# Optimization experiments

Measured on AMD Instinct MI355X. Metric: run time of the kernel, lower is better.

The kernel has to match this reference:

```python
import jax, jax.numpy as jnp
import numpy as np

B, S, D, H = 2, 2048, 1024, 16


def setup_inputs() -> dict:
    key = jax.random.key(0)
    ks = jax.random.split(key, 8)
    wscale = 1.0 / np.sqrt(D)  # ~xavier for square matrices
    return {
        "q": jax.random.normal(ks[0], (B, S, D), jnp.float32),
        "k": jax.random.normal(ks[1], (B, S, D), jnp.float32),
        "v": jax.random.normal(ks[2], (B, S, D), jnp.float32),
        "mask": jnp.tril(jnp.ones((S, S), jnp.int32))[None, None, :, :],  # [1,1,S,S] causal
        "Wq": jax.random.normal(ks[3], (D, D), jnp.float32) * wscale,
        "bq": jnp.zeros((D,), jnp.float32),
        "Wk": jax.random.normal(ks[4], (D, D), jnp.float32) * wscale,
        "bk": jnp.zeros((D,), jnp.float32),
        "Wv": jax.random.normal(ks[5], (D, D), jnp.float32) * wscale,
        "bv": jnp.zeros((D,), jnp.float32),
        "Wo": jax.random.normal(ks[6], (D, D), jnp.float32) * wscale,
        "bo": jnp.zeros((D,), jnp.float32),
    }


def reference(q, k, v, mask, Wq, bq, Wk, bk, Wv, bv, Wo, bo):
    batch_size, seq_len = q.shape[0], q.shape[1]
    qp = q @ Wq + bq
    kp = k @ Wk + bk
    vp = v @ Wv + bv
    qkv = jnp.concatenate([qp, kp, vp], axis=2)          # [B,S,3D]
    qkv = jnp.reshape(qkv, (batch_size, seq_len, H, -1), order='F')  # faithful Fortran-order head split
    qkv = qkv.transpose(0, 2, 1, 3)                      # [B,H,S,3*hd]
    qh, kh, vh = jnp.array_split(qkv, 3, axis=-1)        # each [B,H,S,hd]
    scores = qh @ jnp.swapaxes(kh, -2, -1) / kh.shape[-1] ** 0.5  # [B,H,S,S]
    scores = jnp.where(mask == 0, -9e15, scores)
    attention = jax.nn.softmax(scores, axis=-1)
    values = attention @ vh                              # [B,H,S,hd]
    values = values.transpose(0, 2, 1, 3).reshape(batch_size, seq_len, D)
    out = values @ Wo + bo
    return (out, attention)
```

## Files before the change

kernel.cpp:

```cpp
#include <hip/hip_runtime.h>
#include <stdint.h>

#define B_ 2
#define S_ 2048
#define D_ 1024
#define H_ 16
#define HD_ 64
#define BS_ 4096

typedef __bf16 bf16_t;
typedef __attribute__((ext_vector_type(8))) __bf16 bf16x8;
typedef __attribute__((ext_vector_type(4))) float f32x4;

#define VMCNT0 asm volatile("s_waitcnt vmcnt(0)" ::: "memory")
#define LGKMCNT0 asm volatile("s_waitcnt lgkmcnt(0)" ::: "memory")

__device__ __forceinline__ void barrier_raw() {
  asm volatile("" ::: "memory");
  __builtin_amdgcn_s_barrier();
  asm volatile("" ::: "memory");
}

__device__ __forceinline__ bf16_t f2bf(float f) {
  union { float f; uint32_t u; } v; v.f = f;
  uint32_t r = v.u + 0x7FFFu + ((v.u >> 16) & 1u);
  union { uint16_t u; bf16_t b; } o; o.u = (uint16_t)(r >> 16);
  return o.b;
}

__device__ __forceinline__ void gload_lds16(const void* g, void* l) {
  __builtin_amdgcn_global_load_lds((const __attribute__((address_space(1))) void*)g,
                                   (__attribute__((address_space(3))) void*)l,
                                   16, 0, 0);
}

__device__ __forceinline__ void stage64(const bf16_t* __restrict__ g, int gstride,
                                        bf16_t* lds, int wave, int lane) {
  #pragma unroll
  for (int i = 0; i < 2; ++i) {
    int lin = (wave * 2 + i) * 64 + lane;
    int row = lin >> 3, c = lin & 7;
    gload_lds16(g + (size_t)row * gstride + ((c ^ (row & 7)) << 3), (char*)lds + lin * 16);
  }
}

__device__ __forceinline__ void stage128(const bf16_t* __restrict__ g, int gstride,
                                         bf16_t* lds, int wave, int lane) {
  #pragma unroll
  for (int i = 0; i < 4; ++i) {
    int lin = (wave * 4 + i) * 64 + lane;
    int row = lin >> 3, c = lin & 7;
    gload_lds16(g + (size_t)row * gstride + ((c ^ (row & 7)) << 3), (char*)lds + lin * 16);
  }
}

__device__ __forceinline__ bf16x8 frag64(const bf16_t* lds, int row, int chunk) {
  return *(const bf16x8*)((const char*)lds + row * 128 + ((chunk ^ (row & 7)) << 4));
}

__global__ __launch_bounds__(256) void to_bf16_3_kernel(const float* __restrict__ q,
                                                        const float* __restrict__ k,
                                                        const float* __restrict__ v,
                                                        bf16_t* __restrict__ qb,
                                                        bf16_t* __restrict__ kb,
                                                        bf16_t* __restrict__ vb) {
  const int which = blockIdx.y;
  const float* in = which == 0 ? q : which == 1 ? k : v;
  bf16_t* out = which == 0 ? qb : which == 1 ? kb : vb;
  int i = (blockIdx.x * 256 + threadIdx.x) * 8;
  const float4* p = (const float4*)(in + i);
  float4 a = p[0], b = p[1];
  bf16x8 o;
  o[0] = f2bf(a.x); o[1] = f2bf(a.y); o[2] = f2bf(a.z); o[3] = f2bf(a.w);
  o[4] = f2bf(b.x); o[5] = f2bf(b.y); o[6] = f2bf(b.z); o[7] = f2bf(b.w);
  *(bf16x8*)(out + i) = o;
}

__global__ __launch_bounds__(256) void conv_weight4_kernel(const float* __restrict__ Wq,
                                                           const float* __restrict__ Wk,
                                                           const float* __restrict__ Wv,
                                                           const float* __restrict__ Wo,
                                                           bf16_t* __restrict__ wt_base) {
  const int which = blockIdx.z;
  const float* w = which == 0 ? Wq : which == 1 ? Wk : which == 2 ? Wv : Wo;
  bf16_t* wt = wt_base + (size_t)which * D_ * D_;
  const int permute = (which < 3) ? 1 : 0;
  const float scale = (which == 0) ? 0.125f : 1.0f;

  __shared__ float tile[64][65];
  int d0 = blockIdx.x * 64, o0 = blockIdx.y * 64;
  #pragma unroll
  for (int it = 0; it < 16; ++it) {
    int e = it * 256 + threadIdx.x;
    int r = e >> 6, c = e & 63;
    tile[r][c] = w[(size_t)(d0 + r) * D_ + o0 + c];
  }
  __syncthreads();
  #pragma unroll
  for (int it = 0; it < 16; ++it) {
    int e = it * 256 + threadIdx.x;
    int dd = e & 63, oo = e >> 6;
    int o = o0 + oo;
    int np = permute ? ((o & 15) * 64 + (o >> 4)) : o;
    wt[(size_t)np * D_ + d0 + dd] = f2bf(tile[dd][oo] * scale);
  }
}

__global__ __launch_bounds__(256) void perm_bias_kernel(const float* __restrict__ bq,
                                                        const float* __restrict__ bk,
                                                        const float* __restrict__ bv,
                                                        float* __restrict__ out) {
  int i = blockIdx.x * 256 + threadIdx.x;
  if (i >= 3 * D_) return;
  int which = i >> 10, n = i & 1023;
  int src = (n >> 6) + ((n & 63) << 4);
  const float* b = which == 0 ? bq : (which == 1 ? bk : bv);
  out[i] = b[src] * (which == 0 ? 0.125f : 1.0f);
}

__global__ __launch_bounds__(256) void gemm_qkv_kernel(const bf16_t* __restrict__ Aq,
                                                       const bf16_t* __restrict__ Ak,
                                                       const bf16_t* __restrict__ Av,
                                                       const bf16_t* __restrict__ Bt,
                                                       const float* __restrict__ bias,
                                                       bf16_t* __restrict__ Oq,
                                                       bf16_t* __restrict__ Ok,
                                                       bf16_t* __restrict__ Ov) {
  __shared__ bf16_t As[128 * 64];
  __shared__ bf16_t Bs[128 * 64];
  const int tid = threadIdx.x, wave = tid >> 6, lane = tid & 63;
  const int wm = wave >> 1, wn = wave & 1;
  const int lrow = lane & 15, kgrp = lane >> 4;
  const int row0 = blockIdx.x * 128;
  const int which = blockIdx.y >> 3;
  const int col0 = (blockIdx.y & 7) * 128;
  const bf16_t* A = which == 0 ? Aq : which == 1 ? Ak : Av;
  bf16_t* O = which == 0 ? Oq : which == 1 ? Ok : Ov;
  const bf16_t* Brow = Bt + (size_t)(which * 1024 + col0) * 1024;
  const float* bs = bias + which * 1024 + col0;

  f32x4 acc[4][4];
  #pragma unroll
  for (int i = 0; i < 4; ++i)
    #pragma unroll
    for (int j = 0; j < 4; ++j) acc[i][j] = (f32x4){0.f, 0.f, 0.f, 0.f};

  for (int k0 = 0; k0 < 1024; k0 += 64) {
    __syncthreads();
    stage128(A + (size_t)row0 * 1024 + k0, 1024, As, wave, lane);
    stage128(Brow + k0, 1024, Bs, wave, lane);
    VMCNT0;
    __syncthreads();
    #pragma unroll
    for (int kk = 0; kk < 2; ++kk) {
      bf16x8 af[4], bfv[4];
      #pragma unroll
      for (int mi = 0; mi < 4; ++mi) af[mi] = frag64(As, wm * 64 + mi * 16 + lrow, kk * 4 + kgrp);
      #pragma unroll
      for (int nj = 0; nj < 4; ++nj) bfv[nj] = frag64(Bs, wn * 64 + nj * 16 + lrow, kk * 4 + kgrp);
      #pragma unroll
      for (int mi = 0; mi < 4; ++mi)
        #pragma unroll
        for (int nj = 0; nj < 4; ++nj)
          acc[mi][nj] = __builtin_amdgcn_mfma_f32_16x16x32_bf16(af[mi], bfv[nj], acc[mi][nj], 0, 0, 0);
    }
  }

  #pragma unroll
  for (int mi = 0; mi < 4; ++mi)
    #pragma unroll
    for (int nj = 0; nj < 4; ++nj) {
      const int col = wn * 64 + nj * 16 + lrow;
      const float bv = bs[col];
      #pragma unroll
      for (int r = 0; r < 4; ++r) {
        const int row = row0 + wm * 64 + mi * 16 + kgrp * 4 + r;
        O[(size_t)row * 1024 + col0 + col] = f2bf(acc[mi][nj][r] + bv);
      }
    }
}

__global__ __launch_bounds__(256) void gemm_out_kernel(const bf16_t* __restrict__ A,
                                                       const bf16_t* __restrict__ Bt,
                                                       const float* __restrict__ bias,
                                                       float* __restrict__ Cout) {
  __shared__ bf16_t As[128 * 64];
  __shared__ bf16_t Bs[64 * 64];
  const int tid = threadIdx.x, wave = tid >> 6, lane = tid & 63;
  const int wm = wave >> 1, wn = wave & 1;
  const int lrow = lane & 15, kgrp = lane >> 4;
  const int row0 = blockIdx.x * 128;
  const int col0 = blockIdx.y * 64;

  f32x4 acc[4][2];
  #pragma unroll
  for (int i = 0; i < 4; ++i)
    #pragma unroll
    for (int j = 0; j < 2; ++j) acc[i][j] = (f32x4){0.f, 0.f, 0.f, 0.f};

  for (int k0 = 0; k0 < 1024; k0 += 64) {
    __syncthreads();
    stage128(A + (size_t)row0 * 1024 + k0, 1024, As, wave, lane);
    stage64(Bt + (size_t)col0 * 1024 + k0, 1024, Bs, wave, lane);
    VMCNT0;
    __syncthreads();
    #pragma unroll
    for (int kk = 0; kk < 2; ++kk) {
      bf16x8 af[4], bfv[2];
      #pragma unroll
      for (int mi = 0; mi < 4; ++mi) af[mi] = frag64(As, wm * 64 + mi * 16 + lrow, kk * 4 + kgrp);
      #pragma unroll
      for (int nj = 0; nj < 2; ++nj) bfv[nj] = frag64(Bs, wn * 32 + nj * 16 + lrow, kk * 4 + kgrp);
      #pragma unroll
      for (int mi = 0; mi < 4; ++mi)
        #pragma unroll
        for (int nj = 0; nj < 2; ++nj)
          acc[mi][nj] = __builtin_amdgcn_mfma_f32_16x16x32_bf16(af[mi], bfv[nj], acc[mi][nj], 0, 0, 0);
    }
  }

  #pragma unroll
  for (int mi = 0; mi < 4; ++mi)
    #pragma unroll
    for (int nj = 0; nj < 2; ++nj) {
      const int col = col0 + wn * 32 + nj * 16 + lrow;
      const float bv = bias[col];
      #pragma unroll
      for (int r = 0; r < 4; ++r) {
        const int row = row0 + wm * 64 + mi * 16 + kgrp * 4 + r;
        Cout[(size_t)row * 1024 + col] = acc[mi][nj][r] + bv;
      }
    }
}

__global__ __launch_bounds__(256) void transpose_v_kernel(const bf16_t* __restrict__ Vp,
                                                          bf16_t* __restrict__ Vt) {
  __shared__ bf16_t t[64][80];
  const int st = blockIdx.x, bh = blockIdx.y;
  const int b = bh >> 4, h = bh & 15;
  const int tid = threadIdx.x;
  #pragma unroll
  for (int i = 0; i < 2; ++i) {
    int lin = i * 256 + tid;
    int r = lin >> 3, c = (lin & 7) * 8;
    bf16x8 v8 = *(const bf16x8*)(Vp + ((size_t)(b * S_ + st * 64 + r)) * D_ + h * HD_ + c);
    *(bf16x8*)&t[r][c] = v8;
  }
  __syncthreads();
  #pragma unroll
  for (int i = 0; i < 2; ++i) {
    int lin = i * 256 + tid;
    int f = lin >> 3, c = (lin & 7) * 8;
    bf16x8 o;
    #pragma unroll
    for (int e = 0; e < 8; ++e) o[e] = t[c + e][f];
    *(bf16x8*)(Vt + ((size_t)bh * HD_ + f) * S_ + st * 64 + c) = o;
  }
}

__global__ __launch_bounds__(256) void attn_kernel(const bf16_t* __restrict__ Q,
                                                   const bf16_t* __restrict__ K,
                                                   const bf16_t* __restrict__ Vt,
                                                   float* __restrict__ attn_out,
                                                   bf16_t* __restrict__ values) {
  __shared__ bf16_t Qs[64 * 64];
  __shared__ bf16_t KsB[2][64 * 64];
  __shared__ bf16_t VtsB[2][64 * 64];
  __shared__ bf16_t Ps[4][16 * 72];

  const int tid = threadIdx.x;
  const int wave = tid >> 6, lane = tid & 63;
  const int lrow = lane & 15, kgrp = lane >> 4;
  const int bh = blockIdx.y, b = bh >> 4, h = bh & 15;
  const size_t base = (size_t)b * S_ * D_ + (size_t)h * HD_;
  const size_t vbase = (size_t)bh * HD_ * S_;

  #pragma unroll 1
  for (int half = 0; half < 2; ++half) {
    const int qt = (half == 0) ? (int)blockIdx.x : 31 - (int)blockIdx.x;
    const int qr0 = qt * 64;

    barrier_raw();
    stage64(Q + base + (size_t)qr0 * D_, D_, Qs, wave, lane);
    stage64(K + base, D_, KsB[0], wave, lane);
    VMCNT0; barrier_raw();

    bf16x8 aq[2];
    #pragma unroll
    for (int kk = 0; kk < 2; ++kk) aq[kk] = frag64(Qs, wave * 16 + lrow, kk * 4 + kgrp);

    float psum[4] = {0.f, 0.f, 0.f, 0.f};
    for (int kj = 0; kj <= qt; ++kj) {
      if (kj < qt) stage64(K + base + (size_t)(kj + 1) * 64 * D_, D_, KsB[(kj + 1) & 1], wave, lane);
      const bf16_t* Kc = KsB[kj & 1];
      f32x4 s[4];
      #pragma unroll
      for (int nj = 0; nj < 4; ++nj) {
        s[nj] = (f32x4){0.f, 0.f, 0.f, 0.f};
        #pragma unroll
        for (int kk = 0; kk < 2; ++kk)
          s[nj] = __builtin_amdgcn_mfma_f32_16x16x32_bf16(
              aq[kk], frag64(Kc, nj * 16 + lrow, kk * 4 + kgrp), s[nj], 0, 0, 0);
      }
      if (kj == qt) {
        #pragma unroll
        for (int nj = 0; nj < 4; ++nj)
          #pragma unroll
          for (int r = 0; r < 4; ++r) {
            int lrq = wave * 16 + kgrp * 4 + r;
            int lck = nj * 16 + lrow;
            psum[r] += (lck > lrq) ? 0.f : __expf(s[nj][r]);
          }
      } else {
        #pragma unroll
        for (int nj = 0; nj < 4; ++nj)
          #pragma unroll
          for (int r = 0; r < 4; ++r) psum[r] += __expf(s[nj][r]);
      }
      VMCNT0; barrier_raw();
    }

    float rl[4];
    #pragma unroll
    for (int r = 0; r < 4; ++r) {
      float t = psum[r];
      #pragma unroll
      for (int off = 1; off < 16; off <<= 1) t += __shfl_xor(t, off);
      rl[r] = 1.0f / t;
    }

    f32x4 o[4];
    #pragma unroll
    for (int nj = 0; nj < 4; ++nj) o[nj] = (f32x4){0.f, 0.f, 0.f, 0.f};

    stage64(K + base, D_, KsB[0], wave, lane);
    stage64(Vt + vbase, S_, VtsB[0], wave, lane);
    VMCNT0; barrier_raw();

    for (int kj = 0; kj <= qt; ++kj) {
      if (kj < qt) {
        stage64(K + base + (size_t)(kj + 1) * 64 * D_, D_, KsB[(kj + 1) & 1], wave, lane);
        stage64(Vt + vbase + (kj + 1) * 64, S_, VtsB[(kj + 1) & 1], wave, lane);
      }
      __builtin_amdgcn_sched_barrier(0);
      const bf16_t* Kc = KsB[kj & 1];
      const bf16_t* Vc = VtsB[kj & 1];
      f32x4 s[4];
      #pragma unroll
      for (int nj = 0; nj < 4; ++nj) {
        s[nj] = (f32x4){0.f, 0.f, 0.f, 0.f};
        #pragma unroll
        for (int kk = 0; kk < 2; ++kk)
          s[nj] = __builtin_amdgcn_mfma_f32_16x16x32_bf16(
              aq[kk], frag64(Kc, nj * 16 + lrow, kk * 4 + kgrp), s[nj], 0, 0, 0);
      }
      float* gpb = attn_out + ((size_t)bh * S_ + qr0 + wave * 16 + kgrp * 4) * S_ + kj * 64;
      #pragma unroll
      for (int nj = 0; nj < 4; ++nj)
        #pragma unroll
        for (int r = 0; r < 4; ++r) {
          int lrq = wave * 16 + kgrp * 4 + r;
          int lck = nj * 16 + lrow;
          float p = __expf(s[nj][r]) * rl[r];
          if (kj == qt && lck > lrq) p = 0.f;
          gpb[(size_t)r * S_ + nj * 16 + lrow] = p;
          Ps[wave][(kgrp * 4 + r) * 72 + nj * 16 + lrow] = f2bf(p);
        }
      LGKMCNT0;

      bf16x8 pa[2];
      #pragma unroll
      for (int kk = 0; kk < 2; ++kk)
        pa[kk] = *(const bf16x8*)((const char*)&Ps[wave][0] + lrow * 144 + (kk * 4 + kgrp) * 16);
      #pragma unroll
      for (int nj = 0; nj < 4; ++nj)
        #pragma unroll
        for (int kk = 0; kk < 2; ++kk)
          o[nj] = __builtin_amdgcn_mfma_f32_16x16x32_bf16(
              pa[kk], frag64(Vc, nj * 16 + lrow, kk * 4 + kgrp), o[nj], 0, 0, 0);

      asm volatile("s_waitcnt vmcnt(16)" ::: "memory");
      barrier_raw();
    }

    {
      const int cstart = (qt + 1) * 64;
      if (cstart < S_) {
        int r = tid >> 2;
        float4 z = make_float4(0.f, 0.f, 0.f, 0.f);
        float* rowp = attn_out + ((size_t)bh * S_ + qr0 + r) * S_;
        for (int c = cstart + (tid & 3) * 4; c < S_; c += 16) *(float4*)(rowp + c) = z;
      }
    }

    #pragma unroll
    for (int nj = 0; nj < 4; ++nj)
      #pragma unroll
      for (int r = 0; r < 4; ++r) {
        int grow = qr0 + wave * 16 + kgrp * 4 + r;
        values[(size_t)(b * S_ + grow) * D_ + h * HD_ + nj * 16 + lrow] = f2bf(o[nj][r]);
      }
  }
}

extern "C" void kernel_launch(void* const* d_in, const int* in_sizes, int n_in,
                              void* d_out, int out_size, void* d_ws, size_t ws_size,
                              hipStream_t stream) {
  const float* q  = (const float*)d_in[0];
  const float* k  = (const float*)d_in[1];
  const float* v  = (const float*)d_in[2];
  const float* Wq = (const float*)d_in[4];
  const float* bq = (const float*)d_in[5];
  const float* Wk = (const float*)d_in[6];
  const float* bk = (const float*)d_in[7];
  const float* Wv = (const float*)d_in[8];
  const float* bv = (const float*)d_in[9];
  const float* Wo = (const float*)d_in[10];
  const float* bo = (const float*)d_in[11];

  char* ws = (char*)d_ws;
  bf16_t* qb    = (bf16_t*)ws;
  bf16_t* kb    = qb + (size_t)BS_ * D_;
  bf16_t* vb    = kb + (size_t)BS_ * D_;
  bf16_t* Wqt   = vb + (size_t)BS_ * D_;
  bf16_t* Wkt   = Wqt + (size_t)D_ * D_;
  bf16_t* Wvt   = Wkt + (size_t)D_ * D_;
  bf16_t* Wot   = Wvt + (size_t)D_ * D_;
  float*  bias3 = (float*)(Wot + (size_t)D_ * D_);
  bf16_t* Qp    = (bf16_t*)(bias3 + 3 * D_);
  bf16_t* Kp    = Qp + (size_t)BS_ * D_;
  bf16_t* Vp    = Kp + (size_t)BS_ * D_;
  bf16_t* Vt    = qb;
  bf16_t* Val   = kb;

  to_bf16_3_kernel<<<dim3(2048, 3), 256, 0, stream>>>(q, k, v, qb, kb, vb);
  conv_weight4_kernel<<<dim3(16, 16, 4), 256, 0, stream>>>(Wq, Wk, Wv, Wo, Wqt);
  perm_bias_kernel<<<12, 256, 0, stream>>>(bq, bk, bv, bias3);

  gemm_qkv_kernel<<<dim3(32, 24), 256, 0, stream>>>(qb, kb, vb, Wqt, bias3, Qp, Kp, Vp);
  transpose_v_kernel<<<dim3(32, 32), 256, 0, stream>>>(Vp, Vt);

  float* attn_out = (float*)d_out + (size_t)BS_ * D_;
  attn_kernel<<<dim3(16, 32), 256, 0, stream>>>(Qp, Kp, Vt, attn_out, Val);

  gemm_out_kernel<<<dim3(32, 16), 256, 0, stream>>>(Val, Wot, bo, (float*)d_out);
}
```

Before: 326.8 us.

## Load attention K/V fragments directly to registers and use exp2 with folded scale

The attention kernel no longer stages Q, K and V^T tiles through shared memory with block barriers. Each wave now loads its MFMA fragments straight from global memory into double-buffered registers, and the PV accumulate is software-pipelined one step behind the score computation. The Q weight and bias scale is changed to fold log2(e), so exp2 can replace expf. This removes LDS traffic and barrier stalls, at the cost of more VGPRs and redundant global loads across the four waves, which share K/V only through the cache.

Measured after the change: 413.1 us. 1.26x slower.

```diff
diff --git a/kernel.cpp b/kernel.cpp
--- a/kernel.cpp
+++ b/kernel.cpp
@@ -15,11 +15,7 @@
 #define VMCNT0 asm volatile("s_waitcnt vmcnt(0)" ::: "memory")
 #define LGKMCNT0 asm volatile("s_waitcnt lgkmcnt(0)" ::: "memory")
 
-__device__ __forceinline__ void barrier_raw() {
-  asm volatile("" ::: "memory");
-  __builtin_amdgcn_s_barrier();
-  asm volatile("" ::: "memory");
-}
+#define EXP2F(x) __builtin_amdgcn_exp2f(x)
 
 __device__ __forceinline__ bf16_t f2bf(float f) {
   union { float f; uint32_t u; } v; v.f = f;
@@ -85,7 +81,7 @@
   const float* w = which == 0 ? Wq : which == 1 ? Wk : which == 2 ? Wv : Wo;
   bf16_t* wt = wt_base + (size_t)which * D_ * D_;
   const int permute = (which < 3) ? 1 : 0;
-  const float scale = (which == 0) ? 0.125f : 1.0f;
+  const float scale = (which == 0) ? 0.18033688f : 1.0f;
 
   __shared__ float tile[64][65];
   int d0 = blockIdx.x * 64, o0 = blockIdx.y * 64;
@@ -115,7 +111,7 @@
   int which = i >> 10, n = i & 1023;
   int src = (n >> 6) + ((n & 63) << 4);
   const float* b = which == 0 ? bq : (which == 1 ? bk : bv);
-  out[i] = b[src] * (which == 0 ? 0.125f : 1.0f);
+  out[i] = b[src] * (which == 0 ? 0.18033688f : 1.0f);
 }
 
 __global__ __launch_bounds__(256) void gemm_qkv_kernel(const bf16_t* __restrict__ Aq,
@@ -263,63 +259,100 @@
                                                    const bf16_t* __restrict__ Vt,
                                                    float* __restrict__ attn_out,
                                                    bf16_t* __restrict__ values) {
-  __shared__ bf16_t Qs[64 * 64];
-  __shared__ bf16_t KsB[2][64 * 64];
-  __shared__ bf16_t VtsB[2][64 * 64];
   __shared__ bf16_t Ps[4][16 * 72];
-
   const int tid = threadIdx.x;
   const int wave = tid >> 6, lane = tid & 63;
   const int lrow = lane & 15, kgrp = lane >> 4;
   const int bh = blockIdx.y, b = bh >> 4, h = bh & 15;
   const size_t base = (size_t)b * S_ * D_ + (size_t)h * HD_;
   const size_t vbase = (size_t)bh * HD_ * S_;
+  bf16_t* psw = &Ps[wave][0];
+
+#define LDK(kj_, kf_)                                                          \
+  {                                                                            \
+    const bf16_t* p_ = kp + (size_t)(kj_) * 64 * D_;                           \
+    _Pragma("unroll") for (int nj = 0; nj < 4; ++nj) {                         \
+      kf_[nj * 2] = *(const bf16x8*)(p_ + (size_t)nj * 16 * D_);               \
+      kf_[nj * 2 + 1] = *(const bf16x8*)(p_ + (size_t)nj * 16 * D_ + 32);      \
+    }                                                                          \
+  }
+#define LDV(kj_, vf_)                                                          \
+  {                                                                            \
+    const bf16_t* p_ = vp + (kj_) * 64;                                        \
+    _Pragma("unroll") for (int nj = 0; nj < 4; ++nj) {                         \
+      vf_[nj * 2] = *(const bf16x8*)(p_ + (size_t)nj * 16 * S_);               \
+      vf_[nj * 2 + 1] = *(const bf16x8*)(p_ + (size_t)nj * 16 * S_ + 32);      \
+    }                                                                          \
+  }
+#define QKS(kf_)                                                               \
+  _Pragma("unroll") for (int nj = 0; nj < 4; ++nj) {                           \
+    s[nj] = (f32x4){0.f, 0.f, 0.f, 0.f};                                       \
+    s[nj] = __builtin_amdgcn_mfma_f32_16x16x32_bf16(aq0, kf_[nj * 2], s[nj], 0, 0, 0); \
+    s[nj] = __builtin_amdgcn_mfma_f32_16x16x32_bf16(aq1, kf_[nj * 2 + 1], s[nj], 0, 0, 0); \
+  }
+#define P1BODY(kf_, kj_)                                                       \
+  {                                                                            \
+    f32x4 s[4];                                                                \
+    QKS(kf_)                                                                   \
+    _Pragma("unroll") for (int nj = 0; nj < 4; ++nj)                           \
+      _Pragma("unroll") for (int r = 0; r < 4; ++r) {                          \
+        float e = EXP2F(s[nj][r]);                                             \
+        if ((kj_) == qt && (nj * 16 + lrow) > (wave * 16 + kgrp * 4 + r)) e = 0.f; \
+        psum[r] += e;                                                          \
+      }                                                                        \
+  }
+#define PVACC(vf_)                                                             \
+  {                                                                            \
+    LGKMCNT0;                                                                  \
+    bf16x8 pa0 = *(const bf16x8*)((const char*)psw + lrow * 144 + kgrp * 16);  \
+    bf16x8 pa1 = *(const bf16x8*)((const char*)psw + lrow * 144 + (4 + kgrp) * 16); \
+    _Pragma("unroll") for (int nj = 0; nj < 4; ++nj) {                         \
+      o[nj] = __builtin_amdgcn_mfma_f32_16x16x32_bf16(pa0, vf_[nj * 2], o[nj], 0, 0, 0); \
+      o[nj] = __builtin_amdgcn_mfma_f32_16x16x32_bf16(pa1, vf_[nj * 2 + 1], o[nj], 0, 0, 0); \
+    }                                                                          \
+  }
+#define P2BODY(kc_, kn_, vc_, vn_, kj_)                                        \
+  {                                                                            \
+    if ((kj_) < qt) LDK((kj_) + 1, kn_);                                       \
+    LDV((kj_), vn_);                                                           \
+    f32x4 s[4];                                                                \
+    QKS(kc_)                                                                   \
+    if ((kj_) > 0) PVACC(vc_)                                                  \
+    float* gpb = attn_out + ((size_t)bh * S_ + qr0 + wave * 16 + kgrp * 4) * S_ + (kj_) * 64; \
+    _Pragma("unroll") for (int nj = 0; nj < 4; ++nj)                           \
+      _Pragma("unroll") for (int r = 0; r < 4; ++r) {                          \
+        float p = EXP2F(s[nj][r]) * rl[r];                                     \
+        if ((kj_) == qt && (nj * 16 + lrow) > (wave * 16 + kgrp * 4 + r)) p = 0.f; \
+        gpb[(size_t)r * S_ + nj * 16 + lrow] = p;                              \
+        psw[(kgrp * 4 + r) * 72 + nj * 16 + lrow] = f2bf(p);                   \
+      }                                                                        \
+  }
 
   #pragma unroll 1
   for (int half = 0; half < 2; ++half) {
     const int qt = (half == 0) ? (int)blockIdx.x : 31 - (int)blockIdx.x;
     const int qr0 = qt * 64;
 
-    barrier_raw();
-    stage64(Q + base + (size_t)qr0 * D_, D_, Qs, wave, lane);
-    stage64(K + base, D_, KsB[0], wave, lane);
-    VMCNT0; barrier_raw();
-
-    bf16x8 aq[2];
-    #pragma unroll
-    for (int kk = 0; kk < 2; ++kk) aq[kk] = frag64(Qs, wave * 16 + lrow, kk * 4 + kgrp);
+    const bf16_t* qp = Q + base + (size_t)(qr0 + wave * 16 + lrow) * D_ + kgrp * 8;
+    bf16x8 aq0 = *(const bf16x8*)qp;
+    bf16x8 aq1 = *(const bf16x8*)(qp + 32);
+    const bf16_t* kp = K + base + (size_t)lrow * D_ + kgrp * 8;
+    const bf16_t* vp = Vt + vbase + (size_t)lrow * S_ + kgrp * 8;
 
     float psum[4] = {0.f, 0.f, 0.f, 0.f};
-    for (int kj = 0; kj <= qt; ++kj) {
-      if (kj < qt) stage64(K + base + (size_t)(kj + 1) * 64 * D_, D_, KsB[(kj + 1) & 1], wave, lane);
-      const bf16_t* Kc = KsB[kj & 1];
-      f32x4 s[4];
-      #pragma unroll
-      for (int nj = 0; nj < 4; ++nj) {
-        s[nj] = (f32x4){0.f, 0.f, 0.f, 0.f};
-        #pragma unroll
-        for (int kk = 0; kk < 2; ++kk)
-          s[nj] = __builtin_amdgcn_mfma_f32_16x16x32_bf16(
-              aq[kk], frag64(Kc, nj * 16 + lrow, kk * 4 + kgrp), s[nj], 0, 0, 0);
-      }
-      if (kj == qt) {
-        #pragma unroll
-        for (int nj = 0; nj < 4; ++nj)
-          #pragma unroll
-          for (int r = 0; r < 4; ++r) {
-            int lrq = wave * 16 + kgrp * 4 + r;
-            int lck = nj * 16 + lrow;
-            psum[r] += (lck > lrq) ? 0.f : __expf(s[nj][r]);
-          }
-      } else {
-        #pragma unroll
-        for (int nj = 0; nj < 4; ++nj)
-          #pragma unroll
-          for (int r = 0; r < 4; ++r) psum[r] += __expf(s[nj][r]);
-      }
-      VMCNT0; barrier_raw();
-    }
-
+    {
+      bf16x8 kA[8], kB[8];
+      LDK(0, kA);
+      int kj = 0;
+      while (true) {
+        if (kj < qt) LDK(kj + 1, kB);
+        P1BODY(kA, kj);
+        if (++kj > qt) break;
+        if (kj < qt) LDK(kj + 1, kA);
+        P1BODY(kB, kj);
+        if (++kj > qt) break;
+      }
+    }
     float rl[4];
     #pragma unroll
     for (int r = 0; r < 4; ++r) {
@@ -332,55 +365,17 @@
     f32x4 o[4];
     #pragma unroll
     for (int nj = 0; nj < 4; ++nj) o[nj] = (f32x4){0.f, 0.f, 0.f, 0.f};
-
-    stage64(K + base, D_, KsB[0], wave, lane);
-    stage64(Vt + vbase, S_, VtsB[0], wave, lane);
-    VMCNT0; barrier_raw();
-
-    for (int kj = 0; kj <= qt; ++kj) {
-      if (kj < qt) {
-        stage64(K + base + (size_t)(kj + 1) * 64 * D_, D_, KsB[(kj + 1) & 1], wave, lane);
-        stage64(Vt + vbase + (kj + 1) * 64, S_, VtsB[(kj + 1) & 1], wave, lane);
-      }
-      __builtin_amdgcn_sched_barrier(0);
-      const bf16_t* Kc = KsB[kj & 1];
-      const bf16_t* Vc = VtsB[kj & 1];
-      f32x4 s[4];
-      #pragma unroll
-      for (int nj = 0; nj < 4; ++nj) {
-        s[nj] = (f32x4){0.f, 0.f, 0.f, 0.f};
-        #pragma unroll
-        for (int kk = 0; kk < 2; ++kk)
-          s[nj] = __builtin_amdgcn_mfma_f32_16x16x32_bf16(
-              aq[kk], frag64(Kc, nj * 16 + lrow, kk * 4 + kgrp), s[nj], 0, 0, 0);
-      }
-      float* gpb = attn_out + ((size_t)bh * S_ + qr0 + wave * 16 + kgrp * 4) * S_ + kj * 64;
-      #pragma unroll
-      for (int nj = 0; nj < 4; ++nj)
-        #pragma unroll
-        for (int r = 0; r < 4; ++r) {
-          int lrq = wave * 16 + kgrp * 4 + r;
-          int lck = nj * 16 + lrow;
-          float p = __expf(s[nj][r]) * rl[r];
-          if (kj == qt && lck > lrq) p = 0.f;
-          gpb[(size_t)r * S_ + nj * 16 + lrow] = p;
-          Ps[wave][(kgrp * 4 + r) * 72 + nj * 16 + lrow] = f2bf(p);
-        }
-      LGKMCNT0;
-
-      bf16x8 pa[2];
-      #pragma unroll
-      for (int kk = 0; kk < 2; ++kk)
-        pa[kk] = *(const bf16x8*)((const char*)&Ps[wave][0] + lrow * 144 + (kk * 4 + kgrp) * 16);
-      #pragma unroll
-      for (int nj = 0; nj < 4; ++nj)
-        #pragma unroll
-        for (int kk = 0; kk < 2; ++kk)
-          o[nj] = __builtin_amdgcn_mfma_f32_16x16x32_bf16(
-              pa[kk], frag64(Vc, nj * 16 + lrow, kk * 4 + kgrp), o[nj], 0, 0, 0);
-
-      asm volatile("s_waitcnt vmcnt(16)" ::: "memory");
-      barrier_raw();
+    {
+      bf16x8 kA[8], kB[8], vA[8], vB[8];
+      LDK(0, kA);
+      int kj = 0;
+      while (true) {
+        P2BODY(kA, kB, vA, vB, kj);
+        if (++kj > qt) break;
+        P2BODY(kB, kA, vB, vA, kj);
+        if (++kj > qt) break;
+      }
+      if (qt & 1) { PVACC(vA) } else { PVACC(vB) }
     }
 
     {
@@ -401,6 +396,12 @@
         values[(size_t)(b * S_ + grow) * D_ + h * HD_ + nj * 16 + lrow] = f2bf(o[nj][r]);
       }
   }
+#undef LDK
+#undef LDV
+#undef QKS
+#undef P1BODY
+#undef PVACC
+#undef P2BODY
 }
 
 extern "C" void kernel_launch(void* const* d_in, const int* in_sizes, int n_in,
```

## Split attention into parallel row-sum pass and separate PV pass with exp2

Applied to the files above, without the earlier changes.

Splits the attention kernel into two launches. The first computes the softmax row sums over two interleaved key splits per query tile, writing partial sums to a workspace buffer. The second reads those sums and computes probabilities, writes the attention matrix and accumulates P·V, with one query tile per block instead of two paired tiles. The Q scale is folded with log2(e) so the kernel can use the hardware exp2 instruction, and Q fragments load straight from global memory instead of through LDS. The aim is more blocks for better occupancy and load balance, at the cost of an extra launch, a partial-sum buffer, and losing the paired-tile causal balancing in the PV pass.

Result: slower. 368.5 us (+12.8%).

```diff
diff --git a/kernel.cpp b/kernel.cpp
--- a/kernel.cpp
+++ b/kernel.cpp
@@ -14,6 +14,7 @@
 
 #define VMCNT0 asm volatile("s_waitcnt vmcnt(0)" ::: "memory")
 #define LGKMCNT0 asm volatile("s_waitcnt lgkmcnt(0)" ::: "memory")
+#define EXP2F(x) __builtin_amdgcn_exp2f(x)
 
 __device__ __forceinline__ void barrier_raw() {
   asm volatile("" ::: "memory");
@@ -85,7 +86,7 @@
   const float* w = which == 0 ? Wq : which == 1 ? Wk : which == 2 ? Wv : Wo;
   bf16_t* wt = wt_base + (size_t)which * D_ * D_;
   const int permute = (which < 3) ? 1 : 0;
-  const float scale = (which == 0) ? 0.125f : 1.0f;
+  const float scale = (which == 0) ? 0.18033688f : 1.0f;
 
   __shared__ float tile[64][65];
   int d0 = blockIdx.x * 64, o0 = blockIdx.y * 64;
@@ -115,7 +116,7 @@
   int which = i >> 10, n = i & 1023;
   int src = (n >> 6) + ((n & 63) << 4);
   const float* b = which == 0 ? bq : (which == 1 ? bk : bv);
-  out[i] = b[src] * (which == 0 ? 0.125f : 1.0f);
+  out[i] = b[src] * (which == 0 ? 0.18033688f : 1.0f);
 }
 
 __global__ __launch_bounds__(256) void gemm_qkv_kernel(const bf16_t* __restrict__ Aq,
@@ -258,149 +259,157 @@
   }
 }
 
-__global__ __launch_bounds__(256) void attn_kernel(const bf16_t* __restrict__ Q,
-                                                   const bf16_t* __restrict__ K,
-                                                   const bf16_t* __restrict__ Vt,
-                                                   float* __restrict__ attn_out,
-                                                   bf16_t* __restrict__ values) {
-  __shared__ bf16_t Qs[64 * 64];
+__global__ __launch_bounds__(256) void attn_sum_kernel(const bf16_t* __restrict__ Q,
+                                                       const bf16_t* __restrict__ K,
+                                                       float* __restrict__ part) {
+  __shared__ bf16_t KsB[2][64 * 64];
+  const int tid = threadIdx.x, wave = tid >> 6, lane = tid & 63;
+  const int lrow = lane & 15, kgrp = lane >> 4;
+  const int qt = blockIdx.x, bh = blockIdx.y, ks = blockIdx.z;
+  const int b = bh >> 4, h = bh & 15;
+  const size_t base = (size_t)b * S_ * D_ + (size_t)h * HD_;
+  const int qr0 = qt * 64;
+
+  float psum[4] = {0.f, 0.f, 0.f, 0.f};
+  if (ks <= qt) {
+    const bf16_t* qp = Q + base + (size_t)(qr0 + wave * 16 + lrow) * D_ + kgrp * 8;
+    bf16x8 aq0 = *(const bf16x8*)qp;
+    bf16x8 aq1 = *(const bf16x8*)(qp + 32);
+
+    stage64(K + base + (size_t)ks * 64 * D_, D_, KsB[0], wave, lane);
+    VMCNT0; barrier_raw();
+    for (int kj = ks; kj <= qt; kj += 2) {
+      const int cur = ((kj - ks) >> 1) & 1;
+      if (kj + 2 <= qt)
+        stage64(K + base + (size_t)(kj + 2) * 64 * D_, D_, KsB[cur ^ 1], wave, lane);
+      const bf16_t* Kc = KsB[cur];
+      f32x4 s[4];
+      #pragma unroll
+      for (int nj = 0; nj < 4; ++nj) {
+        s[nj] = (f32x4){0.f, 0.f, 0.f, 0.f};
+        s[nj] = __builtin_amdgcn_mfma_f32_16x16x32_bf16(aq0, frag64(Kc, nj * 16 + lrow, kgrp), s[nj], 0, 0, 0);
+        s[nj] = __builtin_amdgcn_mfma_f32_16x16x32_bf16(aq1, frag64(Kc, nj * 16 + lrow, 4 + kgrp), s[nj], 0, 0, 0);
+      }
+      #pragma unroll
+      for (int nj = 0; nj < 4; ++nj)
+        #pragma unroll
+        for (int r = 0; r < 4; ++r) {
+          float e = EXP2F(s[nj][r]);
+          if (kj == qt && (nj * 16 + lrow) > (wave * 16 + kgrp * 4 + r)) e = 0.f;
+          psum[r] += e;
+        }
+      VMCNT0; barrier_raw();
+    }
+  }
+  #pragma unroll
+  for (int r = 0; r < 4; ++r) {
+    float t = psum[r];
+    #pragma unroll
+    for (int off = 1; off < 16; off <<= 1) t += __shfl_xor(t, off);
+    psum[r] = t;
+  }
+  if (lrow == 0) {
+    #pragma unroll
+    for (int r = 0; r < 4; ++r)
+      part[(size_t)ks * 32 * S_ + (size_t)bh * S_ + qr0 + wave * 16 + kgrp * 4 + r] = psum[r];
+  }
+}
+
+__global__ __launch_bounds__(256) void attn_pv_kernel(const bf16_t* __restrict__ Q,
+                                                      const bf16_t* __restrict__ K,
+                                                      const bf16_t* __restrict__ Vt,
+                                                      const float* __restrict__ part,
+                                                      float* __restrict__ attn_out,
+                                                      bf16_t* __restrict__ values) {
   __shared__ bf16_t KsB[2][64 * 64];
   __shared__ bf16_t VtsB[2][64 * 64];
   __shared__ bf16_t Ps[4][16 * 72];
-
-  const int tid = threadIdx.x;
-  const int wave = tid >> 6, lane = tid & 63;
+  const int tid = threadIdx.x, wave = tid >> 6, lane = tid & 63;
   const int lrow = lane & 15, kgrp = lane >> 4;
+  const int qt = 31 - (int)blockIdx.x;
   const int bh = blockIdx.y, b = bh >> 4, h = bh & 15;
   const size_t base = (size_t)b * S_ * D_ + (size_t)h * HD_;
   const size_t vbase = (size_t)bh * HD_ * S_;
-
-  #pragma unroll 1
-  for (int half = 0; half < 2; ++half) {
-    const int qt = (half == 0) ? (int)blockIdx.x : 31 - (int)blockIdx.x;
-    const int qr0 = qt * 64;
-
+  const int qr0 = qt * 64;
+  bf16_t* psw = &Ps[wave][0];
+
+  float rl[4];
+  {
+    const float* pp = part + (size_t)bh * S_ + qr0 + wave * 16 + kgrp * 4;
+    #pragma unroll
+    for (int r = 0; r < 4; ++r) rl[r] = 1.0f / (pp[r] + *(pp + (size_t)32 * S_ + r));
+  }
+  const bf16_t* qp = Q + base + (size_t)(qr0 + wave * 16 + lrow) * D_ + kgrp * 8;
+  bf16x8 aq0 = *(const bf16x8*)qp;
+  bf16x8 aq1 = *(const bf16x8*)(qp + 32);
+
+  stage64(K + base, D_, KsB[0], wave, lane);
+  stage64(Vt + vbase, S_, VtsB[0], wave, lane);
+  VMCNT0; barrier_raw();
+
+  f32x4 o[4];
+  #pragma unroll
+  for (int nj = 0; nj < 4; ++nj) o[nj] = (f32x4){0.f, 0.f, 0.f, 0.f};
+
+  for (int kj = 0; kj <= qt; ++kj) {
+    const int cur = kj & 1;
+    if (kj < qt) {
+      stage64(K + base + (size_t)(kj + 1) * 64 * D_, D_, KsB[cur ^ 1], wave, lane);
+      stage64(Vt + vbase + (kj + 1) * 64, S_, VtsB[cur ^ 1], wave, lane);
+    }
+    __builtin_amdgcn_sched_barrier(0);
+    const bf16_t* Kc = KsB[cur];
+    const bf16_t* Vc = VtsB[cur];
+    f32x4 s[4];
+    __builtin_amdgcn_s_setprio(1);
+    #pragma unroll
+    for (int nj = 0; nj < 4; ++nj) {
+      s[nj] = (f32x4){0.f, 0.f, 0.f, 0.f};
+      s[nj] = __builtin_amdgcn_mfma_f32_16x16x32_bf16(aq0, frag64(Kc, nj * 16 + lrow, kgrp), s[nj], 0, 0, 0);
+      s[nj] = __builtin_amdgcn_mfma_f32_16x16x32_bf16(aq1, frag64(Kc, nj * 16 + lrow, 4 + kgrp), s[nj], 0, 0, 0);
+    }
+    __builtin_amdgcn_s_setprio(0);
+    float* gpb = attn_out + ((size_t)bh * S_ + qr0 + wave * 16 + kgrp * 4) * S_ + kj * 64;
+    #pragma unroll
+    for (int nj = 0; nj < 4; ++nj)
+      #pragma unroll
+      for (int r = 0; r < 4; ++r) {
+        float p = EXP2F(s[nj][r]) * rl[r];
+        if (kj == qt && (nj * 16 + lrow) > (wave * 16 + kgrp * 4 + r)) p = 0.f;
+        gpb[(size_t)r * S_ + nj * 16 + lrow] = p;
+        psw[(kgrp * 4 + r) * 72 + nj * 16 + lrow] = f2bf(p);
+      }
+    LGKMCNT0;
+    bf16x8 pa0 = *(const bf16x8*)((const char*)psw + lrow * 144 + kgrp * 16);
+    bf16x8 pa1 = *(const bf16x8*)((const char*)psw + lrow * 144 + (4 + kgrp) * 16);
+    __builtin_amdgcn_s_setprio(1);
+    #pragma unroll
+    for (int nj = 0; nj < 4; ++nj) {
+      o[nj] = __builtin_amdgcn_mfma_f32_16x16x32_bf16(pa0, frag64(Vc, nj * 16 + lrow, kgrp), o[nj], 0, 0, 0);
+      o[nj] = __builtin_amdgcn_mfma_f32_16x16x32_bf16(pa1, frag64(Vc, nj * 16 + lrow, 4 + kgrp), o[nj], 0, 0, 0);
+    }
+    __builtin_amdgcn_s_setprio(0);
+    asm volatile("s_waitcnt vmcnt(16)" ::: "memory");
     barrier_raw();
-    stage64(Q + base + (size_t)qr0 * D_, D_, Qs, wave, lane);
-    stage64(K + base, D_, KsB[0], wave, lane);
-    VMCNT0; barrier_raw();
-
-    bf16x8 aq[2];
-    #pragma unroll
-    for (int kk = 0; kk < 2; ++kk) aq[kk] = frag64(Qs, wave * 16 + lrow, kk * 4 + kgrp);
-
-    float psum[4] = {0.f, 0.f, 0.f, 0.f};
-    for (int kj = 0; kj <= qt; ++kj) {
-      if (kj < qt) stage64(K + base + (size_t)(kj + 1) * 64 * D_, D_, KsB[(kj + 1) & 1], wave, lane);
-      const bf16_t* Kc = KsB[kj & 1];
-      f32x4 s[4];
-      #pragma unroll
-      for (int nj = 0; nj < 4; ++nj) {
-        s[nj] = (f32x4){0.f, 0.f, 0.f, 0.f};
-        #pragma unroll
-        for (int kk = 0; kk < 2; ++kk)
-          s[nj] = __builtin_amdgcn_mfma_f32_16x16x32_bf16(
-              aq[kk], frag64(Kc, nj * 16 + lrow, kk * 4 + kgrp), s[nj], 0, 0, 0);
-      }
-      if (kj == qt) {
-        #pragma unroll
-        for (int nj = 0; nj < 4; ++nj)
-          #pragma unroll
-          for (int r = 0; r < 4; ++r) {
-            int lrq = wave * 16 + kgrp * 4 + r;
-            int lck = nj * 16 + lrow;
-            psum[r] += (lck > lrq) ? 0.f : __expf(s[nj][r]);
-          }
-      } else {
-        #pragma unroll
-        for (int nj = 0; nj < 4; ++nj)
-          #pragma unroll
-          for (int r = 0; r < 4; ++r) psum[r] += __expf(s[nj][r]);
-      }
-      VMCNT0; barrier_raw();
-    }
-
-    float rl[4];
+  }
+
+  {
+    const int cstart = (qt + 1) * 64;
+    if (cstart < S_) {
+      int r = tid >> 2;
+      float4 z = make_float4(0.f, 0.f, 0.f, 0.f);
+      float* rowp = attn_out + ((size_t)bh * S_ + qr0 + r) * S_;
+      for (int c = cstart + (tid & 3) * 4; c < S_; c += 16) *(float4*)(rowp + c) = z;
+    }
+  }
+
+  #pragma unroll
+  for (int nj = 0; nj < 4; ++nj)
     #pragma unroll
     for (int r = 0; r < 4; ++r) {
-      float t = psum[r];
-      #pragma unroll
-      for (int off = 1; off < 16; off <<= 1) t += __shfl_xor(t, off);
-      rl[r] = 1.0f / t;
-    }
-
-    f32x4 o[4];
-    #pragma unroll
-    for (int nj = 0; nj < 4; ++nj) o[nj] = (f32x4){0.f, 0.f, 0.f, 0.f};
-
-    stage64(K + base, D_, KsB[0], wave, lane);
-    stage64(Vt + vbase, S_, VtsB[0], wave, lane);
-    VMCNT0; barrier_raw();
-
-    for (int kj = 0; kj <= qt; ++kj) {
-      if (kj < qt) {
-        stage64(K + base + (size_t)(kj + 1) * 64 * D_, D_, KsB[(kj + 1) & 1], wave, lane);
-        stage64(Vt + vbase + (kj + 1) * 64, S_, VtsB[(kj + 1) & 1], wave, lane);
-      }
-      __builtin_amdgcn_sched_barrier(0);
-      const bf16_t* Kc = KsB[kj & 1];
-      const bf16_t* Vc = VtsB[kj & 1];
-      f32x4 s[4];
-      #pragma unroll
-      for (int nj = 0; nj < 4; ++nj) {
-        s[nj] = (f32x4){0.f, 0.f, 0.f, 0.f};
-        #pragma unroll
-        for (int kk = 0; kk < 2; ++kk)
-          s[nj] = __builtin_amdgcn_mfma_f32_16x16x32_bf16(
-              aq[kk], frag64(Kc, nj * 16 + lrow, kk * 4 + kgrp), s[nj], 0, 0, 0);
-      }
-      float* gpb = attn_out + ((size_t)bh * S_ + qr0 + wave * 16 + kgrp * 4) * S_ + kj * 64;
-      #pragma unroll
-      for (int nj = 0; nj < 4; ++nj)
-        #pragma unroll
-        for (int r = 0; r < 4; ++r) {
-          int lrq = wave * 16 + kgrp * 4 + r;
-          int lck = nj * 16 + lrow;
-          float p = __expf(s[nj][r]) * rl[r];
-          if (kj == qt && lck > lrq) p = 0.f;
-          gpb[(size_t)r * S_ + nj * 16 + lrow] = p;
-          Ps[wave][(kgrp * 4 + r) * 72 + nj * 16 + lrow] = f2bf(p);
-        }
-      LGKMCNT0;
-
-      bf16x8 pa[2];
-      #pragma unroll
-      for (int kk = 0; kk < 2; ++kk)
-        pa[kk] = *(const bf16x8*)((const char*)&Ps[wave][0] + lrow * 144 + (kk * 4 + kgrp) * 16);
-      #pragma unroll
-      for (int nj = 0; nj < 4; ++nj)
-        #pragma unroll
-        for (int kk = 0; kk < 2; ++kk)
-          o[nj] = __builtin_amdgcn_mfma_f32_16x16x32_bf16(
-              pa[kk], frag64(Vc, nj * 16 + lrow, kk * 4 + kgrp), o[nj], 0, 0, 0);
-
-      asm volatile("s_waitcnt vmcnt(16)" ::: "memory");
-      barrier_raw();
-    }
-
-    {
-      const int cstart = (qt + 1) * 64;
-      if (cstart < S_) {
-        int r = tid >> 2;
-        float4 z = make_float4(0.f, 0.f, 0.f, 0.f);
-        float* rowp = attn_out + ((size_t)bh * S_ + qr0 + r) * S_;
-        for (int c = cstart + (tid & 3) * 4; c < S_; c += 16) *(float4*)(rowp + c) = z;
-      }
-    }
-
-    #pragma unroll
-    for (int nj = 0; nj < 4; ++nj)
-      #pragma unroll
-      for (int r = 0; r < 4; ++r) {
-        int grow = qr0 + wave * 16 + kgrp * 4 + r;
-        values[(size_t)(b * S_ + grow) * D_ + h * HD_ + nj * 16 + lrow] = f2bf(o[nj][r]);
-      }
-  }
+      int grow = qr0 + wave * 16 + kgrp * 4 + r;
+      values[(size_t)(b * S_ + grow) * D_ + h * HD_ + nj * 16 + lrow] = f2bf(o[nj][r]);
+    }
 }
 
 extern "C" void kernel_launch(void* const* d_in, const int* in_sizes, int n_in,
@@ -430,6 +439,7 @@
   bf16_t* Qp    = (bf16_t*)(bias3 + 3 * D_);
   bf16_t* Kp    = Qp + (size_t)BS_ * D_;
   bf16_t* Vp    = Kp + (size_t)BS_ * D_;
+  float*  part  = (float*)(Vp + (size_t)BS_ * D_);
   bf16_t* Vt    = qb;
   bf16_t* Val   = kb;
 
@@ -441,7 +451,8 @@
   transpose_v_kernel<<<dim3(32, 32), 256, 0, stream>>>(Vp, Vt);
 
   float* attn_out = (float*)d_out + (size_t)BS_ * D_;
-  attn_kernel<<<dim3(16, 32), 256, 0, stream>>>(Qp, Kp, Vt, attn_out, Val);
+  attn_sum_kernel<<<dim3(32, 32, 2), 256, 0, stream>>>(Qp, Kp, part);
+  attn_pv_kernel<<<dim3(32, 32), 256, 0, stream>>>(Qp, Kp, Vt, part, attn_out, Val);
 
   gemm_out_kernel<<<dim3(32, 16), 256, 0, stream>>>(Val, Wot, bo, (float*)d_out);
 }
```
